# Optimization experiments

Hardware: AMD Instinct MI355X
Metric: run time of the kernel (lower is better)

The kernel has to match this reference:

```python
import jax, jax.numpy as jnp
import numpy as np

M, K, N = 1024, 8192, 8192
PACK = 16  # 16 two-bit codes per int32 word


def _pack_ternary(codes):
    # codes: (N, K) int32 with values in {0,1,3} -> (N, K//16) int32
    c = codes.reshape(N, K // PACK, PACK).astype(jnp.uint32)
    shifts = (jnp.arange(PACK, dtype=jnp.uint32) * 2)
    packed = jnp.sum(c << shifts, axis=-1, dtype=jnp.uint32)
    return jax.lax.bitcast_convert_type(packed, jnp.int32)


def setup_inputs() -> dict:
    key = jax.random.key(0)
    kx, kw, kb = jax.random.split(key, 3)
    x = jax.random.normal(kx, (M, K), dtype=jnp.float16)
    # ternary codes drawn from {0,1,3} (code 2 is unused by the format)
    vals = jnp.array([0, 1, 3], dtype=jnp.int32)
    codes = vals[jax.random.randint(kw, (N, K), 0, 3)]
    packed_w = _pack_ternary(codes)
    bias = jax.random.normal(kb, (N,), dtype=jnp.float16)
    return {"x": x, "packed_w": packed_w, "bias": bias}


def _unpack(packed_w):
    # (N, K//16) int32 -> (N, K) fp16 weights with values in {0,1,3}
    shifts = jnp.arange(PACK, dtype=jnp.int32) * 2
    w = (packed_w[:, :, None] >> shifts) & 3  # mask keeps low 2 bits even with arithmetic shift
    return w.reshape(packed_w.shape[0], -1).astype(jnp.float16)


def reference(x, packed_w, bias):
    w = _unpack(packed_w)  # (N, K)
    # Y = X W^T + b, fp32 accumulation as in the CUDA/Triton GEMM, fp16 output
    y = jnp.einsum('mk,nk->mn', x, w, preferred_element_type=jnp.float32)
    y = y.astype(jnp.float16) + bias
    return y
```

## Files before the change

### kernel.cpp

```cpp
#include <hip/hip_runtime.h>
#include <hip/hip_fp16.h>
#include <stdint.h>

#define M_DIM 1024
#define N_DIM 8192
#define K_DIM 8192
#define KP    (K_DIM / 16)

#define BM 128
#define BN 128
#define BK 64
#define NTHREADS 256
#define A_STRIDE 128
#define B_STRIDE 144

typedef _Float16 half8   __attribute__((ext_vector_type(8)));
typedef __fp16   fp16x2  __attribute__((ext_vector_type(2)));
typedef float    f32x4   __attribute__((ext_vector_type(4)));
typedef float    f32x16  __attribute__((ext_vector_type(16)));

#define AS1(p) ((const __attribute__((address_space(1))) void*)(p))
#define AS3(p) ((__attribute__((address_space(3))) void*)(p))

__device__ __forceinline__ uint32_t cvt2(float a, float b) {
  fp16x2 p = __builtin_amdgcn_cvt_pkrtz(a, b);
  return __builtin_bit_cast(uint32_t, p);
}

__device__ __forceinline__ void unpack_word(uint32_t u, uint32_t out[8]) {
  const uint32_t T = 0x42063C00u;
  uint32_t U0 = u & 0x33333333u;
  uint32_t U1 = (u >> 2) & 0x33333333u;
#pragma unroll
  for (int b = 0; b < 4; ++b) {
    uint32_t lo2 = (U0 >> (8 * b)) & 0xFFu;
    uint32_t hi2 = (U1 >> (8 * b)) & 0xFFu;
    uint32_t sel = ((lo2 | (hi2 << 8)) * 0x1001u) & 0x03030303u;
    uint32_t P = __builtin_amdgcn_perm(0u, T, sel);
    out[2 * b]     = __builtin_amdgcn_perm(P, 0u, 0x05000400u);
    out[2 * b + 1] = __builtin_amdgcn_perm(P, 0u, 0x07000600u);
  }
}

__global__ __launch_bounds__(256)
void cvt_x(const float* __restrict__ x, uint16_t* __restrict__ xh) {
  int i = (blockIdx.x * 256 + threadIdx.x) * 8;
  float4 a = *(const float4*)(x + i);
  float4 b = *(const float4*)(x + i + 4);
  uint4 o;
  o.x = cvt2(a.x, a.y); o.y = cvt2(a.z, a.w);
  o.z = cvt2(b.x, b.y); o.w = cvt2(b.z, b.w);
  *(uint4*)(xh + i) = o;
}

__global__ __launch_bounds__(NTHREADS, 2)
void ternary_gemm_ws(const uint16_t* __restrict__ xh,
                     const int*      __restrict__ pw,
                     const float*    __restrict__ bias,
                     float*          __restrict__ out) {
  __shared__ __align__(16) char AsB[BM * A_STRIDE];
  __shared__ __align__(16) char BsB[BN * B_STRIDE];

  const int tid  = threadIdx.x;
  const int lane = tid & 63;
  const int w    = tid >> 6;
  const int wm   = w >> 1, wn = w & 1;
  const int bid  = blockIdx.x;
  const int bm   = (bid & 7) * BM;
  const int bn   = (bid >> 3) * BN;

  const int ar = lane >> 3;
  const int ac = (lane & 7) ^ ar;
  const char* gA[4];
  char*       lA[4];
#pragma unroll
  for (int q = 0; q < 4; ++q) {
    int row = w * 32 + q * 8 + ar;
    gA[q] = (const char*)xh + (size_t)(bm + row) * (K_DIM * 2) + ac * 16;
    lA[q] = AsB + w * 4096 + q * 1024;
  }

  const int rT = tid >> 1, hT = tid & 1;
  const int2* gB = (const int2*)pw + (size_t)(bn + rT) * (KP / 2) + hT;
  char* dBp[4];
#pragma unroll
  for (int h = 0; h < 4; ++h)
    dBp[h] = BsB + rT * B_STRIDE + (hT * 4 + h) * 16;

  int offA[2][4], offB[2][4];
#pragma unroll
  for (int i = 0; i < 2; ++i) {
#pragma unroll
    for (int ks = 0; ks < 4; ++ks) {
      int c = ks * 2 + (lane >> 5);
      int rowA = wm * 64 + i * 32 + (lane & 31);
      offA[i][ks] = rowA * A_STRIDE + ((c ^ (rowA & 7)) * 16);
      offB[i][ks] = (wn * 64 + i * 32 + (lane & 31)) * B_STRIDE + c * 16;
    }
  }

  f32x16 acc[2][2];
#pragma unroll
  for (int i = 0; i < 2; ++i)
#pragma unroll
    for (int j = 0; j < 2; ++j)
      acc[i][j] = (f32x16)(0.f);

  const int NT = K_DIM / BK;
  int2 wcur = gB[0];

  for (int kt = 0; kt < NT; ++kt) {
    __syncthreads();

#pragma unroll
    for (int q = 0; q < 4; ++q) {
      __builtin_amdgcn_global_load_lds(AS1(gA[q]), AS3(lA[q]), 16, 0, 0);
      gA[q] += BK * 2;
    }

    const int kn = (kt + 1 < NT) ? (kt + 1) : kt;
    int2 wnxt = gB[kn * 2];
    uint32_t o0[8], o1[8];
    unpack_word((uint32_t)wcur.x, o0);
    unpack_word((uint32_t)wcur.y, o1);
    *(uint4*)dBp[0] = make_uint4(o0[0], o0[1], o0[2], o0[3]);
    *(uint4*)dBp[1] = make_uint4(o0[4], o0[5], o0[6], o0[7]);
    *(uint4*)dBp[2] = make_uint4(o1[0], o1[1], o1[2], o1[3]);
    *(uint4*)dBp[3] = make_uint4(o1[4], o1[5], o1[6], o1[7]);

    __syncthreads();

#pragma unroll
    for (int ks = 0; ks < 4; ++ks) {
      half8 af[2], bf[2];
#pragma unroll
      for (int i = 0; i < 2; ++i) af[i] = *(const half8*)(AsB + offA[i][ks]);
#pragma unroll
      for (int j = 0; j < 2; ++j) bf[j] = *(const half8*)(BsB + offB[j][ks]);
#pragma unroll
      for (int i = 0; i < 2; ++i)
#pragma unroll
        for (int j = 0; j < 2; ++j)
          acc[i][j] = __builtin_amdgcn_mfma_f32_32x32x16_f16(af[i], bf[j], acc[i][j], 0, 0, 0);
    }
    wcur = wnxt;
  }

#pragma unroll
  for (int j = 0; j < 2; ++j) {
    int n = bn + wn * 64 + j * 32 + (lane & 31);
    __half hb = __float2half_rn(bias[n]);
#pragma unroll
    for (int i = 0; i < 2; ++i) {
      int mbase = bm + wm * 64 + i * 32 + 4 * (lane >> 5);
#pragma unroll
      for (int reg = 0; reg < 16; ++reg) {
        int m = mbase + (reg & 3) + 8 * (reg >> 2);
        __half hy = __float2half_rn(acc[i][j][reg]);
        out[(size_t)m * N_DIM + n] = __half2float(__hadd(hy, hb));
      }
    }
  }
}

__device__ __forceinline__ uint32_t unpack_pair16(uint32_t u, int p) {
  uint32_t c0 = (u >> (4 * p)) & 3u;
  uint32_t c1 = (u >> (4 * p + 2)) & 3u;
  uint32_t lo = (c0 & 1u) * 0x3C00u + (c0 >> 1) * 0x0600u;
  uint32_t hi = (c1 & 1u) * 0x3C00u + (c1 >> 1) * 0x0600u;
  return lo | (hi << 16);
}

__global__ __launch_bounds__(NTHREADS, 2)
void ternary_gemm(const float* __restrict__ x,
                  const int*   __restrict__ pw,
                  const float* __restrict__ bias,
                  float*       __restrict__ out) {
  __shared__ __align__(16) char AsB[BM * B_STRIDE];
  __shared__ __align__(16) char BsB[BN * B_STRIDE];

  const int tid  = threadIdx.x;
  const int lane = tid & 63;
  const int w    = tid >> 6;
  const int wm   = w >> 1, wn = w & 1;
  const int bid  = blockIdx.x;
  const int bm   = (bid & 7) * BM;
  const int bn   = (bid >> 3) * BN;

  const int rT = tid >> 1, hT = tid & 1;
  const float* gA = x + (size_t)(bm + rT) * K_DIM + hT * 32;
  char* const  lA = AsB + rT * B_STRIDE + hT * 64;
  const int2* gB = (const int2*)pw + (size_t)(bn + rT) * (KP / 2) + hT;
  char* dBp[4];
#pragma unroll
  for (int h = 0; h < 4; ++h)
    dBp[h] = BsB + rT * B_STRIDE + (hT * 4 + h) * 16;

  int offA[4][2], offB[4][2];
#pragma unroll
  for (int i = 0; i < 4; ++i)
#pragma unroll
    for (int ks = 0; ks < 2; ++ks) {
      int c = ks * 4 + (lane >> 4);
      offA[i][ks] = (wm * 64 + i * 16 + (lane & 15)) * B_STRIDE + c * 16;
      offB[i][ks] = (wn * 64 + i * 16 + (lane & 15)) * B_STRIDE + c * 16;
    }

  f32x4 acc[4][4];
#pragma unroll
  for (int i = 0; i < 4; ++i)
#pragma unroll
    for (int j = 0; j < 4; ++j)
      acc[i][j] = (f32x4){0.f, 0.f, 0.f, 0.f};

  const int NT = K_DIM / BK;
  for (int kt = 0; kt < NT; ++kt) {
    __syncthreads();
    int2 wcur = gB[kt * 2];
    float4 av[8];
#pragma unroll
    for (int v = 0; v < 8; ++v) av[v] = *(const float4*)(gA + kt * BK + v * 4);
    uint32_t d0[8], d1[8];
#pragma unroll
    for (int p = 0; p < 8; ++p) d0[p] = unpack_pair16((uint32_t)wcur.x, p);
#pragma unroll
    for (int p = 0; p < 8; ++p) d1[p] = unpack_pair16((uint32_t)wcur.y, p);
    *(uint4*)dBp[0] = make_uint4(d0[0], d0[1], d0[2], d0[3]);
    *(uint4*)dBp[1] = make_uint4(d0[4], d0[5], d0[6], d0[7]);
    *(uint4*)dBp[2] = make_uint4(d1[0], d1[1], d1[2], d1[3]);
    *(uint4*)dBp[3] = make_uint4(d1[4], d1[5], d1[6], d1[7]);
#pragma unroll
    for (int v = 0; v < 4; ++v) {
      uint4 aw;
      aw.x = cvt2(av[2 * v].x, av[2 * v].y);
      aw.y = cvt2(av[2 * v].z, av[2 * v].w);
      aw.z = cvt2(av[2 * v + 1].x, av[2 * v + 1].y);
      aw.w = cvt2(av[2 * v + 1].z, av[2 * v + 1].w);
      *(uint4*)(lA + v * 16) = aw;
    }
    __syncthreads();
#pragma unroll
    for (int ks = 0; ks < 2; ++ks) {
      half8 af[4], bf[4];
#pragma unroll
      for (int i = 0; i < 4; ++i) af[i] = *(const half8*)(AsB + offA[i][ks]);
#pragma unroll
      for (int j = 0; j < 4; ++j) bf[j] = *(const half8*)(BsB + offB[j][ks]);
#pragma unroll
      for (int i = 0; i < 4; ++i)
#pragma unroll
        for (int j = 0; j < 4; ++j)
          acc[i][j] = __builtin_amdgcn_mfma_f32_16x16x32_f16(af[i], bf[j], acc[i][j], 0, 0, 0);
    }
  }
#pragma unroll
  for (int j = 0; j < 4; ++j) {
    int n = bn + wn * 64 + j * 16 + (lane & 15);
    __half hb = __float2half_rn(bias[n]);
#pragma unroll
    for (int i = 0; i < 4; ++i) {
      int m0 = bm + wm * 64 + i * 16 + (lane >> 4) * 4;
#pragma unroll
      for (int r = 0; r < 4; ++r) {
        __half hy = __float2half_rn(acc[i][j][r]);
        out[(size_t)(m0 + r) * N_DIM + n] = __half2float(__hadd(hy, hb));
      }
    }
  }
}

extern "C" void kernel_launch(void* const* d_in, const int* in_sizes, int n_in,
                              void* d_out, int out_size, void* d_ws, size_t ws_size,
                              hipStream_t stream) {
  (void)in_sizes; (void)n_in; (void)out_size;
  const float* x    = (const float*)d_in[0];
  const int*   pwp  = (const int*)d_in[1];
  const float* bias = (const float*)d_in[2];
  float*       outp = (float*)d_out;

  const size_t need = (size_t)M_DIM * K_DIM * 2;
  dim3 grid((M_DIM / BM) * (N_DIM / BN));
  if (ws_size >= need) {
    uint16_t* xh = (uint16_t*)d_ws;
    cvt_x<<<(M_DIM * K_DIM) / (256 * 8), 256, 0, stream>>>(x, xh);
    ternary_gemm_ws<<<grid, NTHREADS, 0, stream>>>(xh, pwp, bias, outp);
  } else {
    ternary_gemm<<<grid, NTHREADS, 0, stream>>>(x, pwp, bias, outp);
  }
}
```

Before: 243.5 us.

## Halve GEMM N-tile to 64 and raise occupancy to four blocks per CU

Measured after the change: 260.6 us. +7.0%, slower.

```diff
diff --git a/kernel.cpp b/kernel.cpp
--- a/kernel.cpp
+++ b/kernel.cpp
@@ -8,7 +8,7 @@
 #define KP    (K_DIM / 16)
 
 #define BM 128
-#define BN 128
+#define BN 64
 #define BK 64
 #define NTHREADS 256
 #define A_STRIDE 128
@@ -53,7 +53,7 @@
   *(uint4*)(xh + i) = o;
 }
 
-__global__ __launch_bounds__(NTHREADS, 2)
+__global__ __launch_bounds__(NTHREADS, 4)
 void ternary_gemm_ws(const uint16_t* __restrict__ xh,
                      const int*      __restrict__ pw,
                      const float*    __restrict__ bias,
@@ -80,34 +80,28 @@
     lA[q] = AsB + w * 4096 + q * 1024;
   }
 
-  const int rT = tid >> 1, hT = tid & 1;
-  const int2* gB = (const int2*)pw + (size_t)(bn + rT) * (KP / 2) + hT;
-  char* dBp[4];
-#pragma unroll
-  for (int h = 0; h < 4; ++h)
-    dBp[h] = BsB + rT * B_STRIDE + (hT * 4 + h) * 16;
-
-  int offA[2][4], offB[2][4];
-#pragma unroll
-  for (int i = 0; i < 2; ++i) {
-#pragma unroll
-    for (int ks = 0; ks < 4; ++ks) {
-      int c = ks * 2 + (lane >> 5);
+  const int rB = tid >> 2, wB = tid & 3;
+  const int* gBw = pw + (size_t)(bn + rB) * KP + wB;
+  char* const dB0 = BsB + rB * B_STRIDE + wB * 32;
+
+  int offA[2][4], offB[4];
+#pragma unroll
+  for (int ks = 0; ks < 4; ++ks) {
+    int c = ks * 2 + (lane >> 5);
+#pragma unroll
+    for (int i = 0; i < 2; ++i) {
       int rowA = wm * 64 + i * 32 + (lane & 31);
       offA[i][ks] = rowA * A_STRIDE + ((c ^ (rowA & 7)) * 16);
-      offB[i][ks] = (wn * 64 + i * 32 + (lane & 31)) * B_STRIDE + c * 16;
-    }
-  }
-
-  f32x16 acc[2][2];
-#pragma unroll
-  for (int i = 0; i < 2; ++i)
-#pragma unroll
-    for (int j = 0; j < 2; ++j)
-      acc[i][j] = (f32x16)(0.f);
+    }
+    offB[ks] = (wn * 32 + (lane & 31)) * B_STRIDE + c * 16;
+  }
+
+  f32x16 acc[2];
+#pragma unroll
+  for (int i = 0; i < 2; ++i) acc[i] = (f32x16)(0.f);
 
   const int NT = K_DIM / BK;
-  int2 wcur = gB[0];
+  uint32_t wcur = *gBw;
 
   for (int kt = 0; kt < NT; ++kt) {
     __syncthreads();
@@ -119,36 +113,27 @@
     }
 
     const int kn = (kt + 1 < NT) ? (kt + 1) : kt;
-    int2 wnxt = gB[kn * 2];
-    uint32_t o0[8], o1[8];
-    unpack_word((uint32_t)wcur.x, o0);
-    unpack_word((uint32_t)wcur.y, o1);
-    *(uint4*)dBp[0] = make_uint4(o0[0], o0[1], o0[2], o0[3]);
-    *(uint4*)dBp[1] = make_uint4(o0[4], o0[5], o0[6], o0[7]);
-    *(uint4*)dBp[2] = make_uint4(o1[0], o1[1], o1[2], o1[3]);
-    *(uint4*)dBp[3] = make_uint4(o1[4], o1[5], o1[6], o1[7]);
+    uint32_t wnxt = gBw[kn * 4];
+    uint32_t o[8];
+    unpack_word(wcur, o);
+    *(uint4*)(dB0)      = make_uint4(o[0], o[1], o[2], o[3]);
+    *(uint4*)(dB0 + 16) = make_uint4(o[4], o[5], o[6], o[7]);
 
     __syncthreads();
 
 #pragma unroll
     for (int ks = 0; ks < 4; ++ks) {
-      half8 af[2], bf[2];
-#pragma unroll
-      for (int i = 0; i < 2; ++i) af[i] = *(const half8*)(AsB + offA[i][ks]);
-#pragma unroll
-      for (int j = 0; j < 2; ++j) bf[j] = *(const half8*)(BsB + offB[j][ks]);
-#pragma unroll
-      for (int i = 0; i < 2; ++i)
-#pragma unroll
-        for (int j = 0; j < 2; ++j)
-          acc[i][j] = __builtin_amdgcn_mfma_f32_32x32x16_f16(af[i], bf[j], acc[i][j], 0, 0, 0);
+      half8 af0 = *(const half8*)(AsB + offA[0][ks]);
+      half8 af1 = *(const half8*)(AsB + offA[1][ks]);
+      half8 bf  = *(const half8*)(BsB + offB[ks]);
+      acc[0] = __builtin_amdgcn_mfma_f32_32x32x16_f16(af0, bf, acc[0], 0, 0, 0);
+      acc[1] = __builtin_amdgcn_mfma_f32_32x32x16_f16(af1, bf, acc[1], 0, 0, 0);
     }
     wcur = wnxt;
   }
 
-#pragma unroll
-  for (int j = 0; j < 2; ++j) {
-    int n = bn + wn * 64 + j * 32 + (lane & 31);
+  {
+    int n = bn + wn * 32 + (lane & 31);
     __half hb = __float2half_rn(bias[n]);
 #pragma unroll
     for (int i = 0; i < 2; ++i) {
@@ -156,7 +141,7 @@
 #pragma unroll
       for (int reg = 0; reg < 16; ++reg) {
         int m = mbase + (reg & 3) + 8 * (reg >> 2);
-        __half hy = __float2half_rn(acc[i][j][reg]);
+        __half hy = __float2half_rn(acc[i][reg]);
         out[(size_t)m * N_DIM + n] = __half2float(__hadd(hy, hb));
       }
     }
@@ -176,16 +161,16 @@
                   const int*   __restrict__ pw,
                   const float* __restrict__ bias,
                   float*       __restrict__ out) {
-  __shared__ __align__(16) char AsB[BM * B_STRIDE];
-  __shared__ __align__(16) char BsB[BN * B_STRIDE];
+  __shared__ __align__(16) char AsB[128 * B_STRIDE];
+  __shared__ __align__(16) char BsB[128 * B_STRIDE];
 
   const int tid  = threadIdx.x;
   const int lane = tid & 63;
   const int w    = tid >> 6;
   const int wm   = w >> 1, wn = w & 1;
   const int bid  = blockIdx.x;
-  const int bm   = (bid & 7) * BM;
-  const int bn   = (bid >> 3) * BN;
+  const int bm   = (bid & 7) * 128;
+  const int bn   = (bid >> 3) * 128;
 
   const int rT = tid >> 1, hT = tid & 1;
   const float* gA = x + (size_t)(bm + rT) * K_DIM + hT * 32;
@@ -279,12 +264,13 @@
   float*       outp = (float*)d_out;
 
   const size_t need = (size_t)M_DIM * K_DIM * 2;
-  dim3 grid((M_DIM / BM) * (N_DIM / BN));
   if (ws_size >= need) {
     uint16_t* xh = (uint16_t*)d_ws;
     cvt_x<<<(M_DIM * K_DIM) / (256 * 8), 256, 0, stream>>>(x, xh);
+    dim3 grid((M_DIM / BM) * (N_DIM / BN));
     ternary_gemm_ws<<<grid, NTHREADS, 0, stream>>>(xh, pwp, bias, outp);
   } else {
+    dim3 grid((M_DIM / 128) * (N_DIM / 128));
     ternary_gemm<<<grid, NTHREADS, 0, stream>>>(x, pwp, bias, outp);
   }
 }
```

## Pre-tile X into MFMA fragment layout and load A directly to registers

Applied to the files above, without the earlier changes.

Result: no change. 239.3 us (-1.8%).

```diff
diff --git a/kernel.cpp b/kernel.cpp
--- a/kernel.cpp
+++ b/kernel.cpp
@@ -11,16 +11,16 @@
 #define BN 128
 #define BK 64
 #define NTHREADS 256
-#define A_STRIDE 128
 #define B_STRIDE 144
+#define B_BUF    (BN * B_STRIDE)
+
+#define MT_STRIDE 2097152
+#define KT_STRIDE 16384
 
 typedef _Float16 half8   __attribute__((ext_vector_type(8)));
 typedef __fp16   fp16x2  __attribute__((ext_vector_type(2)));
 typedef float    f32x4   __attribute__((ext_vector_type(4)));
 typedef float    f32x16  __attribute__((ext_vector_type(16)));
-
-#define AS1(p) ((const __attribute__((address_space(1))) void*)(p))
-#define AS3(p) ((__attribute__((address_space(3))) void*)(p))
 
 __device__ __forceinline__ uint32_t cvt2(float a, float b) {
   fp16x2 p = __builtin_amdgcn_cvt_pkrtz(a, b);
@@ -43,107 +43,137 @@
 }
 
 __global__ __launch_bounds__(256)
-void cvt_x(const float* __restrict__ x, uint16_t* __restrict__ xh) {
-  int i = (blockIdx.x * 256 + threadIdx.x) * 8;
-  float4 a = *(const float4*)(x + i);
-  float4 b = *(const float4*)(x + i + 4);
-  uint4 o;
-  o.x = cvt2(a.x, a.y); o.y = cvt2(a.z, a.w);
-  o.z = cvt2(b.x, b.y); o.w = cvt2(b.z, b.w);
-  *(uint4*)(xh + i) = o;
+void cvt_x_t(const float* __restrict__ x, char* __restrict__ xhT) {
+  __shared__ __align__(16) char st[16384];
+  const int b  = blockIdx.x;
+  const int mt = b >> 7, kt = b & 127;
+  const int t  = threadIdx.x;
+#pragma unroll
+  for (int p = 0; p < 8; ++p) {
+    int f   = t + 256 * p;
+    int R   = f >> 4;
+    int cc4 = f & 15;
+    float4 v = *(const float4*)(x + (size_t)(mt * 128 + R) * K_DIM + kt * 64 + cc4 * 4);
+    uint32_t w0 = cvt2(v.x, v.y), w1 = cvt2(v.z, v.w);
+    int c8 = cc4 >> 1, hh = cc4 & 1;
+    int i32 = R >> 5, r = R & 31, ks = c8 >> 1, q = c8 & 1;
+    *(uint2*)(st + i32 * 4096 + ks * 1024 + q * 512 + r * 16 + hh * 8) = make_uint2(w0, w1);
+  }
+  __syncthreads();
+  char* outb = xhT + (size_t)mt * MT_STRIDE + (size_t)kt * KT_STRIDE;
+#pragma unroll
+  for (int e = 0; e < 4; ++e) {
+    int d = (e * 256 + t) * 16;
+    *(uint4*)(outb + d) = *(const uint4*)(st + d);
+  }
 }
 
 __global__ __launch_bounds__(NTHREADS, 2)
-void ternary_gemm_ws(const uint16_t* __restrict__ xh,
-                     const int*      __restrict__ pw,
-                     const float*    __restrict__ bias,
-                     float*          __restrict__ out) {
-  __shared__ __align__(16) char AsB[BM * A_STRIDE];
-  __shared__ __align__(16) char BsB[BN * B_STRIDE];
+void ternary_gemm_rA(const char* __restrict__ xhT,
+                     const int*  __restrict__ pw,
+                     const float* __restrict__ bias,
+                     float*       __restrict__ out) {
+  __shared__ __align__(16) char BsB[2 * B_BUF];
 
   const int tid  = threadIdx.x;
   const int lane = tid & 63;
   const int w    = tid >> 6;
   const int wm   = w >> 1, wn = w & 1;
   const int bid  = blockIdx.x;
-  const int bm   = (bid & 7) * BM;
+  const int mt   = bid & 7;
+  const int bm   = mt * BM;
   const int bn   = (bid >> 3) * BN;
 
-  const int ar = lane >> 3;
-  const int ac = (lane & 7) ^ ar;
-  const char* gA[4];
-  char*       lA[4];
-#pragma unroll
-  for (int q = 0; q < 4; ++q) {
-    int row = w * 32 + q * 8 + ar;
-    gA[q] = (const char*)xh + (size_t)(bm + row) * (K_DIM * 2) + ac * 16;
-    lA[q] = AsB + w * 4096 + q * 1024;
-  }
+  const char* pA[2];
+#pragma unroll
+  for (int i = 0; i < 2; ++i)
+    pA[i] = xhT + (size_t)mt * MT_STRIDE + (wm * 2 + i) * 4096 + lane * 16;
 
   const int rT = tid >> 1, hT = tid & 1;
   const int2* gB = (const int2*)pw + (size_t)(bn + rT) * (KP / 2) + hT;
-  char* dBp[4];
-#pragma unroll
-  for (int h = 0; h < 4; ++h)
-    dBp[h] = BsB + rT * B_STRIDE + (hT * 4 + h) * 16;
-
-  int offA[2][4], offB[2][4];
-#pragma unroll
-  for (int i = 0; i < 2; ++i) {
+  int dBoff[4];
+#pragma unroll
+  for (int h = 0; h < 4; ++h) dBoff[h] = rT * B_STRIDE + (hT * 4 + h) * 16;
+
+  int offB[2][4];
+#pragma unroll
+  for (int j = 0; j < 2; ++j)
+#pragma unroll
+    for (int ks = 0; ks < 4; ++ks)
+      offB[j][ks] = (wn * 64 + j * 32 + (lane & 31)) * B_STRIDE + (ks * 2 + (lane >> 5)) * 16;
+
+  f32x16 acc[2][2];
+#pragma unroll
+  for (int i = 0; i < 2; ++i)
+#pragma unroll
+    for (int j = 0; j < 2; ++j) acc[i][j] = (f32x16)(0.f);
+
+  const int NT = K_DIM / BK;
+
+  {
+    int2 w0 = gB[0];
+    uint32_t o0[8], o1[8];
+    unpack_word((uint32_t)w0.x, o0);
+    unpack_word((uint32_t)w0.y, o1);
+    *(uint4*)(BsB + dBoff[0]) = make_uint4(o0[0], o0[1], o0[2], o0[3]);
+    *(uint4*)(BsB + dBoff[1]) = make_uint4(o0[4], o0[5], o0[6], o0[7]);
+    *(uint4*)(BsB + dBoff[2]) = make_uint4(o1[0], o1[1], o1[2], o1[3]);
+    *(uint4*)(BsB + dBoff[3]) = make_uint4(o1[4], o1[5], o1[6], o1[7]);
+  }
+  half8 aCur[2][4], aNxt[2][4];
+#pragma unroll
+  for (int i = 0; i < 2; ++i)
+#pragma unroll
+    for (int ks = 0; ks < 4; ++ks)
+      aCur[i][ks] = *(const half8*)(pA[i] + ks * 1024);
+#pragma unroll
+  for (int i = 0; i < 2; ++i) pA[i] += KT_STRIDE;
+  int2 wcur = gB[2];
+  __syncthreads();
+
+  for (int kt = 0; kt < NT; ++kt) {
+    const int cur = kt & 1;
+
+#pragma unroll
+    for (int i = 0; i < 2; ++i)
+#pragma unroll
+      for (int ks = 0; ks < 4; ++ks)
+        aNxt[i][ks] = *(const half8*)(pA[i] + ks * 1024);
+    if (kt < NT - 2) {
+#pragma unroll
+      for (int i = 0; i < 2; ++i) pA[i] += KT_STRIDE;
+    }
+    int kn2 = (kt + 2 < NT) ? (kt + 2) : (NT - 1);
+    int2 wnxt = gB[kn2 * 2];
+
+    const char* bb = BsB + cur * B_BUF;
 #pragma unroll
     for (int ks = 0; ks < 4; ++ks) {
-      int c = ks * 2 + (lane >> 5);
-      int rowA = wm * 64 + i * 32 + (lane & 31);
-      offA[i][ks] = rowA * A_STRIDE + ((c ^ (rowA & 7)) * 16);
-      offB[i][ks] = (wn * 64 + i * 32 + (lane & 31)) * B_STRIDE + c * 16;
-    }
-  }
-
-  f32x16 acc[2][2];
-#pragma unroll
-  for (int i = 0; i < 2; ++i)
-#pragma unroll
-    for (int j = 0; j < 2; ++j)
-      acc[i][j] = (f32x16)(0.f);
-
-  const int NT = K_DIM / BK;
-  int2 wcur = gB[0];
-
-  for (int kt = 0; kt < NT; ++kt) {
+      half8 bf0 = *(const half8*)(bb + offB[0][ks]);
+      half8 bf1 = *(const half8*)(bb + offB[1][ks]);
+      acc[0][0] = __builtin_amdgcn_mfma_f32_32x32x16_f16(aCur[0][ks], bf0, acc[0][0], 0, 0, 0);
+      acc[0][1] = __builtin_amdgcn_mfma_f32_32x32x16_f16(aCur[0][ks], bf1, acc[0][1], 0, 0, 0);
+      acc[1][0] = __builtin_amdgcn_mfma_f32_32x32x16_f16(aCur[1][ks], bf0, acc[1][0], 0, 0, 0);
+      acc[1][1] = __builtin_amdgcn_mfma_f32_32x32x16_f16(aCur[1][ks], bf1, acc[1][1], 0, 0, 0);
+    }
+
+    {
+      char* wb = BsB + (cur ^ 1) * B_BUF;
+      uint32_t o0[8], o1[8];
+      unpack_word((uint32_t)wcur.x, o0);
+      unpack_word((uint32_t)wcur.y, o1);
+      *(uint4*)(wb + dBoff[0]) = make_uint4(o0[0], o0[1], o0[2], o0[3]);
+      *(uint4*)(wb + dBoff[1]) = make_uint4(o0[4], o0[5], o0[6], o0[7]);
+      *(uint4*)(wb + dBoff[2]) = make_uint4(o1[0], o1[1], o1[2], o1[3]);
+      *(uint4*)(wb + dBoff[3]) = make_uint4(o1[4], o1[5], o1[6], o1[7]);
+    }
+
     __syncthreads();
-
-#pragma unroll
-    for (int q = 0; q < 4; ++q) {
-      __builtin_amdgcn_global_load_lds(AS1(gA[q]), AS3(lA[q]), 16, 0, 0);
-      gA[q] += BK * 2;
-    }
-
-    const int kn = (kt + 1 < NT) ? (kt + 1) : kt;
-    int2 wnxt = gB[kn * 2];
-    uint32_t o0[8], o1[8];
-    unpack_word((uint32_t)wcur.x, o0);
-    unpack_word((uint32_t)wcur.y, o1);
-    *(uint4*)dBp[0] = make_uint4(o0[0], o0[1], o0[2], o0[3]);
-    *(uint4*)dBp[1] = make_uint4(o0[4], o0[5], o0[6], o0[7]);
-    *(uint4*)dBp[2] = make_uint4(o1[0], o1[1], o1[2], o1[3]);
-    *(uint4*)dBp[3] = make_uint4(o1[4], o1[5], o1[6], o1[7]);
-
-    __syncthreads();
-
-#pragma unroll
-    for (int ks = 0; ks < 4; ++ks) {
-      half8 af[2], bf[2];
-#pragma unroll
-      for (int i = 0; i < 2; ++i) af[i] = *(const half8*)(AsB + offA[i][ks]);
-#pragma unroll
-      for (int j = 0; j < 2; ++j) bf[j] = *(const half8*)(BsB + offB[j][ks]);
-#pragma unroll
-      for (int i = 0; i < 2; ++i)
-#pragma unroll
-        for (int j = 0; j < 2; ++j)
-          acc[i][j] = __builtin_amdgcn_mfma_f32_32x32x16_f16(af[i], bf[j], acc[i][j], 0, 0, 0);
-    }
     wcur = wnxt;
+#pragma unroll
+    for (int i = 0; i < 2; ++i)
+#pragma unroll
+      for (int ks = 0; ks < 4; ++ks) aCur[i][ks] = aNxt[i][ks];
   }
 
 #pragma unroll
@@ -176,16 +206,16 @@
                   const int*   __restrict__ pw,
                   const float* __restrict__ bias,
                   float*       __restrict__ out) {
-  __shared__ __align__(16) char AsB[BM * B_STRIDE];
-  __shared__ __align__(16) char BsB[BN * B_STRIDE];
+  __shared__ __align__(16) char AsB[128 * B_STRIDE];
+  __shared__ __align__(16) char BsB[128 * B_STRIDE];
 
   const int tid  = threadIdx.x;
   const int lane = tid & 63;
   const int w    = tid >> 6;
   const int wm   = w >> 1, wn = w & 1;
   const int bid  = blockIdx.x;
-  const int bm   = (bid & 7) * BM;
-  const int bn   = (bid >> 3) * BN;
+  const int bm   = (bid & 7) * 128;
+  const int bn   = (bid >> 3) * 128;
 
   const int rT = tid >> 1, hT = tid & 1;
   const float* gA = x + (size_t)(bm + rT) * K_DIM + hT * 32;
@@ -279,12 +309,13 @@
   float*       outp = (float*)d_out;
 
   const size_t need = (size_t)M_DIM * K_DIM * 2;
-  dim3 grid((M_DIM / BM) * (N_DIM / BN));
   if (ws_size >= need) {
-    uint16_t* xh = (uint16_t*)d_ws;
-    cvt_x<<<(M_DIM * K_DIM) / (256 * 8), 256, 0, stream>>>(x, xh);
-    ternary_gemm_ws<<<grid, NTHREADS, 0, stream>>>(xh, pwp, bias, outp);
+    char* xhT = (char*)d_ws;
+    cvt_x_t<<<8 * 128, 256, 0, stream>>>(x, xhT);
+    dim3 grid((M_DIM / BM) * (N_DIM / BN));
+    ternary_gemm_rA<<<grid, NTHREADS, 0, stream>>>(xhT, pwp, bias, outp);
   } else {
+    dim3 grid((M_DIM / 128) * (N_DIM / 128));
     ternary_gemm<<<grid, NTHREADS, 0, stream>>>(x, pwp, bias, outp);
   }
 }
```
